# Kernel optimization log

Hardware: AMD Instinct MI355X
Metric: run time of the kernel (lower is better)

## Reference

```python
import jax, jax.numpy as jnp
import numpy as np

NUM_HEADS = 12


def setup_inputs() -> dict:
    key = jax.random.key(0)
    k1, k2, k3 = jax.random.split(key, 3)
    B, N, C = 2, 2048, 768
    x = jax.random.normal(k1, (B, N, C), dtype=jnp.float32)
    # torch nn.Linear weights: [out_features, in_features]
    w_qkv = jax.random.normal(k2, (3 * C, C), dtype=jnp.float32) * (C ** -0.5)
    w_mlp = jax.random.normal(k3, (C, C), dtype=jnp.float32) * (C ** -0.5)
    b_mlp = jnp.zeros((C,), dtype=jnp.float32)
    return {"x": x, "w_qkv": w_qkv, "w_mlp": w_mlp, "b_mlp": b_mlp}


def reference(x, w_qkv, w_mlp, b_mlp):
    B, N, C = x.shape
    H = NUM_HEADS
    hd = C // H
    scale = hd ** -0.5
    # qkv linear (no bias), then the module's reshape: [B,N,H,3,hd]
    qkv = (x @ w_qkv.T).reshape(B, N, H, 3, hd)
    # permute(3,0,2,1,4) -> q,k,v each [B,H,N,hd]
    q = jnp.transpose(qkv[:, :, :, 0, :], (0, 2, 1, 3))
    k = jnp.transpose(qkv[:, :, :, 1, :], (0, 2, 1, 3))
    v = jnp.transpose(qkv[:, :, :, 2, :], (0, 2, 1, 3))
    attn = jax.nn.softmax(jnp.einsum('bhqd,bhkd->bhqk', q, k) * scale, axis=-1)
    out = jnp.einsum('bhqk,bhkd->bhqd', attn, v)          # [B,H,N,hd]
    out = jnp.transpose(out, (0, 2, 1, 3)).reshape(B, N, C)
    return out @ w_mlp.T + b_mlp
```

## Files before the change

kernel.cpp:

```cpp
#include <hip/hip_runtime.h>
#include <math.h>

typedef unsigned short u16;
typedef unsigned int   u32;
typedef __attribute__((ext_vector_type(8))) short s8v;
typedef __attribute__((ext_vector_type(2))) unsigned int u32x2;
typedef __attribute__((ext_vector_type(4))) float f4v;

#define NHEADS 12
#define SEQ 2048
#define CD 768
#define BB 2
#define QKVD 2304
#define CEXP 0.18033688f
#define DEFER_THR 44.0f

__device__ inline u16 f2bf(float f) {
    union { float f; unsigned u; } v; v.f = f;
    unsigned r = v.u + 0x7FFFu + ((v.u >> 16) & 1u);
    return (u16)(r >> 16);
}
__device__ inline u32 cvtpk_bf16(float lo, float hi) {
    u32 r;
    asm("v_cvt_pk_bf16_f32 %0, %1, %2" : "=v"(r) : "v"(lo), "v"(hi));
    return r;
}
__device__ inline float exp2_fast(float x) {
    float r;
    asm("v_exp_f32 %0, %1" : "=v"(r) : "v"(x));
    return r;
}
__device__ inline float max3f(float a, float b, float c) {
    float r;
    asm("v_max3_f32 %0, %1, %2, %3" : "=v"(r) : "v"(a), "v"(b), "v"(c));
    return r;
}

#define GLOAD16(SRC, DST) __builtin_amdgcn_global_load_lds(                 \
    (const __attribute__((address_space(1))) void*)(SRC),                   \
    (__attribute__((address_space(3))) void*)(DST), 16, 0, 0)

#define SW(r, c) ((((r) << 6) + (c)) ^ (((r) & 7) << 3))

__global__ __launch_bounds__(256)
void cvt3_kernel(const float* __restrict__ a, u16* __restrict__ oa, int na,
                 const float* __restrict__ b, u16* __restrict__ ob, int nb,
                 const float* __restrict__ c, u16* __restrict__ oc) {
    const int i = (blockIdx.x * 256 + threadIdx.x) * 8;
    const float* src; u16* dst;
    if (i < na)           { src = a + i;            dst = oa + i; }
    else if (i < na + nb) { src = b + (i - na);     dst = ob + (i - na); }
    else                  { src = c + (i - na - nb); dst = oc + (i - na - nb); }
    const float4 x = *(const float4*)src;
    const float4 y = *(const float4*)(src + 4);
    s8v o;
    o[0] = (short)f2bf(x.x); o[1] = (short)f2bf(x.y);
    o[2] = (short)f2bf(x.z); o[3] = (short)f2bf(x.w);
    o[4] = (short)f2bf(y.x); o[5] = (short)f2bf(y.y);
    o[6] = (short)f2bf(y.z); o[7] = (short)f2bf(y.w);
    *(s8v*)dst = o;
}

template<int BN, int NBX, bool OUT_BF16, bool BIAS>
__global__ __launch_bounds__(256)
void gemm_bf16(const u16* __restrict__ A, const u16* __restrict__ W,
               const float* __restrict__ bias, void* __restrict__ Cout,
               int M, int N, int K) {
    constexpr int NF = BN / 32;
    __shared__ u16 As[8192];
    __shared__ u16 Bs[BN * 64];
    const int tid = threadIdx.x;
    const int l  = tid & 63, w = tid >> 6;
    const int wr = w >> 1, wc = w & 1;
    const int lq = l & 15, lg = l >> 4;

    const int fid = blockIdx.x;
    const int cpx = gridDim.x >> 3;
    const int swz = (fid & 7) * cpx + (fid >> 3);
    const int rowBase = (swz / NBX) << 7;
    const int colBase = (swz % NBX) * BN;

    f4v acc[4][NF];
    #pragma unroll
    for (int m = 0; m < 4; ++m)
        #pragma unroll
        for (int n = 0; n < NF; ++n)
            #pragma unroll
            for (int r = 0; r < 4; ++r) acc[m][n][r] = 0.f;

    const int chunk = l & 7;
    const int r8    = l >> 3;

    for (int kb = 0; kb < K; kb += 64) {
        __syncthreads();
        #pragma unroll
        for (int j = 0; j < 4; ++j) {
            const int rowA = (w << 5) + (j << 3) + r8;
            const int sc   = (chunk ^ (rowA & 7)) << 3;
            GLOAD16(A + (size_t)(rowBase + rowA) * K + kb + sc,
                    &As[(w << 11) + (j << 9)]);
        }
        #pragma unroll
        for (int j = 0; j < NF; ++j) {
            const int rowB = w * (BN / 4) + (j << 3) + r8;
            const int sc   = (chunk ^ (rowB & 7)) << 3;
            GLOAD16(W + (size_t)(colBase + rowB) * K + kb + sc,
                    &Bs[w * (BN * 16) + (j << 9)]);
        }
        __syncthreads();
        #pragma unroll
        for (int h = 0; h < 2; ++h) {
            const int kc = (h << 5) + (lg << 3);
            s8v af[4], bf[NF];
            #pragma unroll
            for (int m = 0; m < 4; ++m)
                af[m] = *(const s8v*)&As[SW((wr << 6) + (m << 4) + lq, kc)];
            #pragma unroll
            for (int n = 0; n < NF; ++n)
                bf[n] = *(const s8v*)&Bs[SW(wc * (BN / 2) + (n << 4) + lq, kc)];
            #pragma unroll
            for (int m = 0; m < 4; ++m)
                #pragma unroll
                for (int n = 0; n < NF; ++n)
                    acc[m][n] = __builtin_amdgcn_mfma_f32_16x16x32_bf16(
                        af[m], bf[n], acc[m][n], 0, 0, 0);
        }
    }

    #pragma unroll
    for (int m = 0; m < 4; ++m)
        #pragma unroll
        for (int r = 0; r < 4; ++r) {
            const int row = rowBase + (wr << 6) + (m << 4) + (lg << 2) + r;
            #pragma unroll
            for (int n = 0; n < NF; ++n) {
                const int col = colBase + wc * (BN / 2) + (n << 4) + lq;
                float v = acc[m][n][r];
                if (BIAS) v += bias[col];
                if (OUT_BF16) ((u16*)Cout)[(size_t)row * N + col] = f2bf(v);
                else        ((float*)Cout)[(size_t)row * N + col] = v;
            }
        }
}

__global__ __launch_bounds__(256)
void gemm64_bf16(const u16* __restrict__ A, const u16* __restrict__ W,
                 const float* __restrict__ bias, float* __restrict__ C,
                 int M, int N, int K) {
    __shared__ u16 As[4096];
    __shared__ u16 Bs[4096];
    const int tid = threadIdx.x;
    const int l  = tid & 63, w = tid >> 6;
    const int wr = w >> 1, wc = w & 1;
    const int lq = l & 15, lg = l >> 4;

    const int fid = blockIdx.x;
    const int cpx = gridDim.x >> 3;
    const int swz = (fid & 7) * cpx + (fid >> 3);
    const int rowBase = (swz / 12) << 6;
    const int colBase = (swz % 12) << 6;

    f4v acc[2][2];
    #pragma unroll
    for (int m = 0; m < 2; ++m)
        #pragma unroll
        for (int n = 0; n < 2; ++n)
            #pragma unroll
            for (int r = 0; r < 4; ++r) acc[m][n][r] = 0.f;

    const int chunk = l & 7;
    const int r8    = l >> 3;

    for (int kb = 0; kb < K; kb += 64) {
        __syncthreads();
        #pragma unroll
        for (int j = 0; j < 2; ++j) {
            const int rowA = (w << 4) + (j << 3) + r8;
            const int sc   = (chunk ^ (rowA & 7)) << 3;
            GLOAD16(A + (size_t)(rowBase + rowA) * K + kb + sc,
                    &As[(w << 10) + (j << 9)]);
            GLOAD16(W + (size_t)(colBase + rowA) * K + kb + sc,
                    &Bs[(w << 10) + (j << 9)]);
        }
        __syncthreads();
        #pragma unroll
        for (int h = 0; h < 2; ++h) {
            const int kc = (h << 5) + (lg << 3);
            s8v af[2], bf[2];
            #pragma unroll
            for (int m = 0; m < 2; ++m)
                af[m] = *(const s8v*)&As[SW((wr << 5) + (m << 4) + lq, kc)];
            #pragma unroll
            for (int n = 0; n < 2; ++n)
                bf[n] = *(const s8v*)&Bs[SW((wc << 5) + (n << 4) + lq, kc)];
            #pragma unroll
            for (int m = 0; m < 2; ++m)
                #pragma unroll
                for (int n = 0; n < 2; ++n)
                    acc[m][n] = __builtin_amdgcn_mfma_f32_16x16x32_bf16(
                        af[m], bf[n], acc[m][n], 0, 0, 0);
        }
    }

    #pragma unroll
    for (int m = 0; m < 2; ++m)
        #pragma unroll
        for (int r = 0; r < 4; ++r) {
            const int row = rowBase + (wr << 5) + (m << 4) + (lg << 2) + r;
            #pragma unroll
            for (int n = 0; n < 2; ++n) {
                const int col = colBase + (wc << 5) + (n << 4) + lq;
                C[(size_t)row * N + col] = acc[m][n][r] + bias[col];
            }
        }
}

__global__ __launch_bounds__(256)
void vtrans_kernel(const u16* __restrict__ qkvb, u16* __restrict__ vT) {
    __shared__ u16 T[64][66];
    const int bh = blockIdx.y;
    const int tt = blockIdx.x;
    const int b = bh / NHEADS, h = bh % NHEADS;
    const int r  = threadIdx.x >> 2;
    const int dc = (threadIdx.x & 3) << 4;
    const u16* src = qkvb + (size_t)(b * SEQ + tt * 64 + r) * QKVD
                   + h * 192 + 128 + dc;
    *(s8v*)&T[r][dc]     = *(const s8v*)(src);
    *(s8v*)&T[r][dc + 8] = *(const s8v*)(src + 8);
    __syncthreads();
    const int d  = threadIdx.x >> 2;
    const int tc = (threadIdx.x & 3) << 4;
    s8v o0, o1;
    #pragma unroll
    for (int j = 0; j < 8; ++j) {
        o0[j] = (short)T[tc + j][d];
        o1[j] = (short)T[tc + 8 + j][d];
    }
    u16* dst = vT + ((size_t)bh * 64 + d) * SEQ + tt * 64 + tc;
    *(s8v*)dst = o0;
    *(s8v*)(dst + 8) = o1;
}

__global__ __launch_bounds__(512)
void attn_mfma(const u16* __restrict__ qkv, const u16* __restrict__ vT,
               u16* __restrict__ outb) {
    __shared__ u16 SL[24576];
    const int tid = threadIdx.x;
    const int l = tid & 63, w = tid >> 6;
    const int g = w >> 2, wl = w & 3;
    const int lq = l & 15, lg = l >> 4;

    const int fid = blockIdx.x;
    const int swz = (fid & 7) * 96 + (fid >> 3);
    const int q0 = (swz & 31) << 6;
    const int bh = swz >> 5;
    const int b = bh / NHEADS, h = bh % NHEADS;
    const u16* base = qkv + (size_t)b * SEQ * QKVD + h * 192;
    const u16* vbh  = vT + (size_t)bh * 64 * SEQ;
    u16* QP = SL + 16384;
    float* Of32 = (float*)(SL + 8192);
    float* Msh  = (float*)(SL + 16384);
    float* Lsh  = Msh + 64;

    const int kv0 = g << 10;

    u32 koff[2], voff[2], kdst[2], vdst[2];
    {
        const int cs = l & 7;
        #pragma unroll
        for (int i = 0; i < 2; ++i) {
            const int row = (wl << 4) + (i << 3) + (l >> 3);
            koff[i] = (u32)(row * QKVD + 64 + ((cs ^ (row & 7)) << 3));
            voff[i] = (u32)(row * SEQ  +      ((cs ^ (row & 7)) << 3));
            kdst[i] = (u32)((g << 13) + (wl << 10) + (i << 9));
            vdst[i] = (u32)((g << 13) + 4096 + (wl << 10) + (i << 9));
        }
    }

    {
        const u16* sbK = base + (size_t)kv0 * QKVD;
        const u16* sbV = vbh + kv0;
        #pragma unroll
        for (int i = 0; i < 2; ++i) {
            GLOAD16(sbK + koff[i], &SL[kdst[i]]);
            GLOAD16(sbV + voff[i], &SL[vdst[i]]);
        }
    }
    {
        const s8v q1 = *(const s8v*)(base + (size_t)(q0 + l) * QKVD + (w << 3));
        *(s8v*)&QP[SW(l, w << 3)] = q1;
    }
    __syncthreads();
    s8v qf[2];
    #pragma unroll
    for (int h2 = 0; h2 < 2; ++h2)
        qf[h2] = *(const s8v*)&QP[SW((wl << 4) + lq, (h2 << 5) + (lg << 3))];

    s8v onesf;
    {
        const short o = (lq == 0) ? (short)0x3F80 : (short)0;
        #pragma unroll
        for (int e = 0; e < 8; ++e) onesf[e] = o;
    }
    f4v fz;
    #pragma unroll
    for (int r = 0; r < 4; ++r) fz[r] = 0.f;

    f4v oacc[4], osum;
    #pragma unroll
    for (int db = 0; db < 4; ++db)
        #pragma unroll
        for (int r = 0; r < 4; ++r) oacc[db][r] = 0.f;
    #pragma unroll
    for (int r = 0; r < 4; ++r) osum[r] = 0.f;
    float mrun = -3.0e38f;

    const u16* Kc = SL + (g << 13);
    const u16* Vc = Kc + 4096;

    for (int t = 0; t < 16; ++t) {
        __syncthreads();

        float p[16];
        __builtin_amdgcn_s_setprio(1);
        #pragma unroll
        for (int kb = 0; kb < 4; ++kb) {
            const s8v k0 = *(const s8v*)&Kc[SW((kb << 4) + lq, (lg << 3))];
            const s8v k1 = *(const s8v*)&Kc[SW((kb << 4) + lq, 32 + (lg << 3))];
            f4v z;
            z = __builtin_amdgcn_mfma_f32_16x16x32_bf16(k0, qf[0], fz, 0, 0, 0);
            z = __builtin_amdgcn_mfma_f32_16x16x32_bf16(k1, qf[1], z, 0, 0, 0);
            #pragma unroll
            for (int r = 0; r < 4; ++r) p[(kb << 2) + r] = z[r];
        }
        __builtin_amdgcn_s_setprio(0);

        __syncthreads();
        if (t < 15) {
            const u16* sbK = base + (size_t)(kv0 + (t + 1) * 64) * QKVD;
            #pragma unroll
            for (int i = 0; i < 2; ++i)
                GLOAD16(sbK + koff[i], &SL[kdst[i]]);
        }

        float m1_ = max3f(p[0], p[1], p[2]);
        float m2_ = max3f(p[3], p[4], p[5]);
        float m3_ = max3f(p[6], p[7], p[8]);
        float m4_ = max3f(p[9], p[10], p[11]);
        float m5_ = max3f(p[12], p[13], p[14]);
        float mx  = fmaxf(max3f(m1_, m2_, p[15]), max3f(m3_, m4_, m5_));
        if (!__all(mx <= mrun + DEFER_THR)) {
            mx = fmaxf(mx, __shfl_xor(mx, 16));
            mx = fmaxf(mx, __shfl_xor(mx, 32));
            const float mn = fmaxf(mrun, mx);
            const float al = exp2_fast((mrun - mn) * CEXP);
            mrun = mn;
            float ar[4];
            #pragma unroll
            for (int r = 0; r < 4; ++r) ar[r] = __shfl(al, (lg << 2) + r);
            #pragma unroll
            for (int db = 0; db < 4; ++db)
                #pragma unroll
                for (int r = 0; r < 4; ++r) oacc[db][r] *= ar[r];
            #pragma unroll
            for (int r = 0; r < 4; ++r) osum[r] *= ar[r];
        }
        const float mC = -mrun * CEXP;
        #pragma unroll
        for (int i = 0; i < 16; ++i) p[i] = exp2_fast(fmaf(p[i], CEXP, mC));

        #pragma unroll
        for (int kb = 0; kb < 4; ++kb) {
            u32x2 pw;
            pw[0] = cvtpk_bf16(p[(kb << 2) + 0], p[(kb << 2) + 1]);
            pw[1] = cvtpk_bf16(p[(kb << 2) + 2], p[(kb << 2) + 3]);
            *(u32x2*)&QP[SW((w << 4) + lq, (kb << 4) + (lg << 2))] = pw;
        }
        const s8v pf0 = *(const s8v*)&QP[SW((w << 4) + lq, (lg << 3))];
        const s8v pf1 = *(const s8v*)&QP[SW((w << 4) + lq, 32 + (lg << 3))];

        __builtin_amdgcn_s_setprio(1);
        #pragma unroll
        for (int db = 0; db < 4; ++db) {
            const s8v v0 = *(const s8v*)&Vc[SW((db << 4) + lq, (lg << 3))];
            const s8v v1 = *(const s8v*)&Vc[SW((db << 4) + lq, 32 + (lg << 3))];
            oacc[db] = __builtin_amdgcn_mfma_f32_16x16x32_bf16(pf0, v0, oacc[db], 0, 0, 0);
            oacc[db] = __builtin_amdgcn_mfma_f32_16x16x32_bf16(pf1, v1, oacc[db], 0, 0, 0);
        }
        osum = __builtin_amdgcn_mfma_f32_16x16x32_bf16(pf0, onesf, osum, 0, 0, 0);
        osum = __builtin_amdgcn_mfma_f32_16x16x32_bf16(pf1, onesf, osum, 0, 0, 0);
        __builtin_amdgcn_s_setprio(0);

        __syncthreads();
        if (t < 15) {
            const u16* sbV = vbh + kv0 + (t + 1) * 64;
            #pragma unroll
            for (int i = 0; i < 2; ++i)
                GLOAD16(sbV + voff[i], &SL[vdst[i]]);
        }
    }

    if (g == 1) {
        if (lg == 0) Msh[(wl << 4) + lq] = mrun;
        if (lq == 0) {
            #pragma unroll
            for (int r = 0; r < 4; ++r)
                Lsh[(wl << 4) + (lg << 2) + r] = osum[r];
        }
        #pragma unroll
        for (int db = 0; db < 4; ++db)
            #pragma unroll
            for (int r = 0; r < 4; ++r)
                Of32[(((wl << 4) + (lg << 2) + r) << 6) + (db << 4) + lq] =
                    oacc[db][r];
    }
    __syncthreads();
    if (g == 0) {
        #pragma unroll
        for (int r = 0; r < 4; ++r) {
            const int rowq = (wl << 4) + (lg << 2) + r;
            const float m0r = __shfl(mrun, (lg << 2) + r);
            const float l0r = __shfl(osum[r], l & 48);
            const float m1r = Msh[rowq];
            const float l1r = Lsh[rowq];
            const float M   = fmaxf(m0r, m1r);
            const float w0  = exp2_fast((m0r - M) * CEXP);
            const float w1  = exp2_fast((m1r - M) * CEXP);
            const float inv = 1.f / (l0r * w0 + l1r * w1);
            const float a0 = w0 * inv, a1 = w1 * inv;
            const size_t row = (size_t)b * SEQ + q0 + rowq;
            #pragma unroll
            for (int db = 0; db < 4; ++db) {
                const float o1 = Of32[(rowq << 6) + (db << 4) + lq];
                outb[row * CD + h * 64 + (db << 4) + lq] =
                    f2bf(oacc[db][r] * a0 + o1 * a1);
            }
        }
    }
}

extern "C" void kernel_launch(void* const* d_in, const int* in_sizes, int n_in,
                              void* d_out, int out_size, void* d_ws, size_t ws_size,
                              hipStream_t stream) {
    const float* x     = (const float*)d_in[0];
    const float* w_qkv = (const float*)d_in[1];
    const float* w_mlp = (const float*)d_in[2];
    const float* b_mlp = (const float*)d_in[3];
    float* out = (float*)d_out;

    const int NX  = BB * SEQ * CD;
    const int NWQ = QKVD * CD;
    const int NWM = CD * CD;
    const int NQK = BB * SEQ * QKVD;
    const int NAT = BB * SEQ * CD;
    u16* xb    = (u16*)d_ws;
    u16* wqkvb = xb + NX;
    u16* wmlpb = wqkvb + NWQ;
    u16* qkvb  = wmlpb + NWM;
    u16* attnb = qkvb + NQK;
    u16* vTb   = attnb + NAT;

    cvt3_kernel<<<(NX + NWQ + NWM) / 2048, 256, 0, stream>>>(
        x, xb, NX, w_qkv, wqkvb, NWQ, w_mlp, wmlpb);

    const int M = BB * SEQ;
    {
        gemm_bf16<128, 18, true, false><<<576, 256, 0, stream>>>(
            xb, wqkvb, nullptr, qkvb, M, QKVD, CD);
    }
    {
        dim3 grid(SEQ / 64, BB * NHEADS);
        vtrans_kernel<<<grid, 256, 0, stream>>>(qkvb, vTb);
    }
    {
        attn_mfma<<<768, 512, 0, stream>>>(qkvb, vTb, attnb);
    }
    {
        gemm64_bf16<<<768, 256, 0, stream>>>(attnb, wmlpb, b_mlp, out,
                                             M, CD, CD);
    }
}
```

Baseline: 88.76 us.

## Fuse V transpose into QKV GEMM epilogue and retile to 96-wide columns

```diff
diff --git a/kernel.cpp b/kernel.cpp
--- a/kernel.cpp
+++ b/kernel.cpp
@@ -61,14 +61,12 @@
     *(s8v*)dst = o;
 }
 
-template<int BN, int NBX, bool OUT_BF16, bool BIAS>
 __global__ __launch_bounds__(256)
-void gemm_bf16(const u16* __restrict__ A, const u16* __restrict__ W,
-               const float* __restrict__ bias, void* __restrict__ Cout,
-               int M, int N, int K) {
-    constexpr int NF = BN / 32;
+void gemm_qkv(const u16* __restrict__ A, const u16* __restrict__ W,
+              u16* __restrict__ Cout, u16* __restrict__ vT,
+              int M, int N, int K) {
     __shared__ u16 As[8192];
-    __shared__ u16 Bs[BN * 64];
+    __shared__ u16 Bs[6144];
     const int tid = threadIdx.x;
     const int l  = tid & 63, w = tid >> 6;
     const int wr = w >> 1, wc = w & 1;
@@ -77,14 +75,14 @@
     const int fid = blockIdx.x;
     const int cpx = gridDim.x >> 3;
     const int swz = (fid & 7) * cpx + (fid >> 3);
-    const int rowBase = (swz / NBX) << 7;
-    const int colBase = (swz % NBX) * BN;
-
-    f4v acc[4][NF];
+    const int rowBase = (swz / 24) << 7;
+    const int colBase = (swz % 24) * 96;
+
+    f4v acc[4][3];
     #pragma unroll
     for (int m = 0; m < 4; ++m)
         #pragma unroll
-        for (int n = 0; n < NF; ++n)
+        for (int n = 0; n < 3; ++n)
             #pragma unroll
             for (int r = 0; r < 4; ++r) acc[m][n][r] = 0.f;
 
@@ -101,44 +99,59 @@
                     &As[(w << 11) + (j << 9)]);
         }
         #pragma unroll
-        for (int j = 0; j < NF; ++j) {
-            const int rowB = w * (BN / 4) + (j << 3) + r8;
+        for (int j = 0; j < 3; ++j) {
+            const int rowB = w * 24 + (j << 3) + r8;
             const int sc   = (chunk ^ (rowB & 7)) << 3;
             GLOAD16(W + (size_t)(colBase + rowB) * K + kb + sc,
-                    &Bs[w * (BN * 16) + (j << 9)]);
+                    &Bs[w * 1536 + (j << 9)]);
         }
         __syncthreads();
         #pragma unroll
         for (int h = 0; h < 2; ++h) {
             const int kc = (h << 5) + (lg << 3);
-            s8v af[4], bf[NF];
+            s8v af[4], bf[3];
             #pragma unroll
             for (int m = 0; m < 4; ++m)
                 af[m] = *(const s8v*)&As[SW((wr << 6) + (m << 4) + lq, kc)];
             #pragma unroll
-            for (int n = 0; n < NF; ++n)
-                bf[n] = *(const s8v*)&Bs[SW(wc * (BN / 2) + (n << 4) + lq, kc)];
+            for (int n = 0; n < 3; ++n)
+                bf[n] = *(const s8v*)&Bs[SW(wc * 48 + (n << 4) + lq, kc)];
             #pragma unroll
             for (int m = 0; m < 4; ++m)
                 #pragma unroll
-                for (int n = 0; n < NF; ++n)
+                for (int n = 0; n < 3; ++n)
                     acc[m][n] = __builtin_amdgcn_mfma_f32_16x16x32_bf16(
                         af[m], bf[n], acc[m][n], 0, 0, 0);
         }
     }
 
+    const int bb = rowBase >> 11;
+    const int tokBase = (rowBase & 2047) + (wr << 6);
+    bool isV[3]; size_t vb[3];
+    #pragma unroll
+    for (int n = 0; n < 3; ++n) {
+        const int c0 = colBase + wc * 48 + (n << 4);
+        const int cm = c0 % 192;
+        isV[n] = (cm >= 128);
+        const int h = c0 / 192;
+        vb[n] = ((size_t)(((bb * NHEADS + h) << 6) + (cm - 128) + lq)) * SEQ
+              + tokBase;
+    }
     #pragma unroll
     for (int m = 0; m < 4; ++m)
         #pragma unroll
         for (int r = 0; r < 4; ++r) {
             const int row = rowBase + (wr << 6) + (m << 4) + (lg << 2) + r;
-            #pragma unroll
-            for (int n = 0; n < NF; ++n) {
-                const int col = colBase + wc * (BN / 2) + (n << 4) + lq;
-                float v = acc[m][n][r];
-                if (BIAS) v += bias[col];
-                if (OUT_BF16) ((u16*)Cout)[(size_t)row * N + col] = f2bf(v);
-                else        ((float*)Cout)[(size_t)row * N + col] = v;
+            const int toff = (m << 4) + (lg << 2) + r;
+            #pragma unroll
+            for (int n = 0; n < 3; ++n) {
+                const u16 v = f2bf(acc[m][n][r]);
+                if (isV[n]) {
+                    vT[vb[n] + toff] = v;
+                } else {
+                    const int col = colBase + wc * 48 + (n << 4) + lq;
+                    Cout[(size_t)row * N + col] = v;
+                }
             }
         }
 }
@@ -213,32 +226,6 @@
                 C[(size_t)row * N + col] = acc[m][n][r] + bias[col];
             }
         }
-}
-
-__global__ __launch_bounds__(256)
-void vtrans_kernel(const u16* __restrict__ qkvb, u16* __restrict__ vT) {
-    __shared__ u16 T[64][66];
-    const int bh = blockIdx.y;
-    const int tt = blockIdx.x;
-    const int b = bh / NHEADS, h = bh % NHEADS;
-    const int r  = threadIdx.x >> 2;
-    const int dc = (threadIdx.x & 3) << 4;
-    const u16* src = qkvb + (size_t)(b * SEQ + tt * 64 + r) * QKVD
-                   + h * 192 + 128 + dc;
-    *(s8v*)&T[r][dc]     = *(const s8v*)(src);
-    *(s8v*)&T[r][dc + 8] = *(const s8v*)(src + 8);
-    __syncthreads();
-    const int d  = threadIdx.x >> 2;
-    const int tc = (threadIdx.x & 3) << 4;
-    s8v o0, o1;
-    #pragma unroll
-    for (int j = 0; j < 8; ++j) {
-        o0[j] = (short)T[tc + j][d];
-        o1[j] = (short)T[tc + 8 + j][d];
-    }
-    u16* dst = vT + ((size_t)bh * 64 + d) * SEQ + tt * 64 + tc;
-    *(s8v*)dst = o0;
-    *(s8v*)(dst + 8) = o1;
 }
 
 __global__ __launch_bounds__(512)
@@ -465,12 +452,7 @@
 
     const int M = BB * SEQ;
     {
-        gemm_bf16<128, 18, true, false><<<576, 256, 0, stream>>>(
-            xb, wqkvb, nullptr, qkvb, M, QKVD, CD);
-    }
-    {
-        dim3 grid(SEQ / 64, BB * NHEADS);
-        vtrans_kernel<<<grid, 256, 0, stream>>>(qkvb, vTb);
+        gemm_qkv<<<768, 256, 0, stream>>>(xb, wqkvb, qkvb, vTb, M, QKVD, CD);
     }
     {
         attn_mfma<<<768, 512, 0, stream>>>(qkvb, vTb, attnb);
```

New measurement: 90.94 us. +2.5%, slower.
